# Kernel optimization log

Measured on AMD Instinct MI355X. Metric: run time of the kernel, lower is better.

## Reference

```python
import jax, jax.numpy as jnp
import numpy as np

B, T, D, H = 2, 2048, 1024, 16
DK = D // H


def setup_inputs() -> dict:
    key = jax.random.key(0)
    ks = jax.random.split(key, 11)
    s = 0.02
    inp = {
        "q": jax.random.normal(ks[0], (B, T, D), jnp.float32),
        "k": jax.random.normal(ks[1], (B, T, D), jnp.float32),
        "v": jax.random.normal(ks[2], (B, T, D), jnp.float32),
        # True = masked (causal), broadcast over batch and heads
        "attn_mask": jnp.triu(jnp.ones((T, T), bool), k=1)[None, None],
        "Wq": jax.random.normal(ks[3], (D, D), jnp.float32) * s,
        "bq": jnp.zeros((D,), jnp.float32),
        "Wk": jax.random.normal(ks[4], (D, D), jnp.float32) * s,
        "bk": jnp.zeros((D,), jnp.float32),
        "Wv": jax.random.normal(ks[5], (D, D), jnp.float32) * s,
        "bv": jnp.zeros((D,), jnp.float32),
        "Wo": jax.random.normal(ks[6], (D, D), jnp.float32) * s,
        "bo": jnp.zeros((D,), jnp.float32),
    }
    return inp


def _split_heads(x):
    # [B,T,D] -> [B,H,T,DK]
    return x.reshape(B, T, H, DK).transpose(0, 2, 1, 3)


def reference(q, k, v, attn_mask, Wq, bq, Wk, bk, Wv, bv, Wo, bo):
    query = _split_heads(q @ Wq.T + bq)
    key_ = _split_heads(k @ Wk.T + bk)
    value = _split_heads(v @ Wv.T + bv)
    scale = 1.0 / jnp.sqrt(jnp.asarray(DK, query.dtype))
    scores = jnp.einsum("bhqd,bhkd->bhqk", query, key_) * scale
    scores = jnp.where(attn_mask, -jnp.inf, scores)
    probs = jax.nn.softmax(scores, axis=-1)  # dropout p=0.0 (eval)
    ctx = jnp.einsum("bhqk,bhkd->bhqd", probs, value)
    ctx = ctx.transpose(0, 2, 1, 3).reshape(B, T, D)
    return ctx @ Wo.T + bo
```

## Files before the change

### kernel.cpp

```cpp
#include <hip/hip_runtime.h>
#include <stdint.h>

#define Bsz 2
#define Tseq 2048
#define Dmodel 1024
#define Hn 16
#define DKd 64

typedef __bf16 bf16;
typedef bf16 bf16x8 __attribute__((ext_vector_type(8)));
typedef float f32x4 __attribute__((ext_vector_type(4)));

__device__ inline void gld_lds16(const void* g, void* l) {
  __builtin_amdgcn_global_load_lds(
      (const __attribute__((address_space(1))) uint32_t*)g,
      (__attribute__((address_space(3))) uint32_t*)l, 16, 0, 0);
}

struct CvtArgs {
  const float* src[7];
  bf16* dst[7];
  int n4[7];
};

__global__ void __launch_bounds__(256) cvt_f32_bf16(CvtArgs a) {
  const int z = blockIdx.y;
  const float4* s = (const float4*)a.src[z];
  uint2* d = (uint2*)a.dst[z];
  const int n4 = a.n4[z];
  for (int i = blockIdx.x * 256 + threadIdx.x; i < n4; i += gridDim.x * 256) {
    float4 v = s[i];
    union { bf16 h[4]; uint2 u; } pk;
    pk.h[0] = (bf16)v.x; pk.h[1] = (bf16)v.y;
    pk.h[2] = (bf16)v.z; pk.h[3] = (bf16)v.w;
    d[i] = pk.u;
  }
}

struct GemmArgs {
  const bf16* A[3];
  const bf16* W[3];
  const float* bias[3];
  void* out[3];
  int mode[3];
  float scale[3];
};

__global__ void __launch_bounds__(256) gemm_bt(GemmArgs g) {
  const int z = blockIdx.z;
  const bf16* __restrict__ A = g.A[z];
  const bf16* __restrict__ W = g.W[z];
  const float* __restrict__ bias = g.bias[z];
  const int mode = g.mode[z];
  const float scl = g.scale[z];

  __shared__ __align__(16) bf16 As[128 * 32];
  __shared__ __align__(16) bf16 Bs[128 * 32];

  const int tid = threadIdx.x;
  const int w = tid >> 6, lane = tid & 63;
  const int l15 = lane & 15, quad = lane >> 4;
  const int wm = (w >> 1) * 64, wn = (w & 1) * 64;
  const int m0 = blockIdx.y * 128, n0 = blockIdx.x * 128;

  f32x4 zero = {0.f, 0.f, 0.f, 0.f};
  f32x4 acc[4][4];
#pragma unroll
  for (int mi = 0; mi < 4; ++mi)
#pragma unroll
    for (int ni = 0; ni < 4; ++ni) acc[mi][ni] = zero;

  for (int k0 = 0; k0 < Dmodel; k0 += 32) {
    __syncthreads();
#pragma unroll
    for (int p = 0; p < 2; ++p) {
      const int c = p * 256 + tid;
      const int row = c >> 2, ko = (c & 3) * 8;
      gld_lds16(A + (size_t)(m0 + row) * Dmodel + k0 + ko, (void*)(As + c * 8));
      gld_lds16(W + (size_t)(n0 + row) * Dmodel + k0 + ko, (void*)(Bs + c * 8));
    }
    __syncthreads();

    bf16x8 af[4], bfr[4];
#pragma unroll
    for (int i = 0; i < 4; ++i) {
      af[i]  = *(const bf16x8*)(As + (wm + i * 16 + l15) * 32 + quad * 8);
      bfr[i] = *(const bf16x8*)(Bs + (wn + i * 16 + l15) * 32 + quad * 8);
    }
#pragma unroll
    for (int mi = 0; mi < 4; ++mi)
#pragma unroll
      for (int ni = 0; ni < 4; ++ni)
        acc[mi][ni] = __builtin_amdgcn_mfma_f32_16x16x32_bf16(af[mi], bfr[ni],
                                                              acc[mi][ni], 0, 0, 0);
  }

#pragma unroll
  for (int mi = 0; mi < 4; ++mi) {
#pragma unroll
    for (int r = 0; r < 4; ++r) {
      const int m = m0 + wm + mi * 16 + quad * 4 + r;
      const int bb = m >> 11, tt = m & 2047;
#pragma unroll
      for (int ni = 0; ni < 4; ++ni) {
        const int n = n0 + wn + ni * 16 + l15;
        const float val = (acc[mi][ni][r] + bias[n]) * scl;
        if (mode == 0) {
          bf16* o = (bf16*)g.out[z];
          const int hh = n >> 6, dk = n & 63;
          o[((size_t)(bb * Hn + hh) * Tseq + tt) * DKd + dk] = (bf16)val;
        } else if (mode == 1) {
          bf16* o = (bf16*)g.out[z];
          const int hh = n >> 6, dk = n & 63;
          o[((size_t)(bb * Hn + hh) * DKd + dk) * Tseq + tt] = (bf16)val;
        } else {
          float* o = (float*)g.out[z];
          o[(size_t)m * Dmodel + n] = val;
        }
      }
    }
  }
}

__global__ void __launch_bounds__(256) gemm_out64(const bf16* __restrict__ A,
                                                  const bf16* __restrict__ W,
                                                  const float* __restrict__ bias,
                                                  float* __restrict__ out) {
  __shared__ __align__(16) bf16 As[64 * 32];
  __shared__ __align__(16) bf16 Bs[128 * 32];

  const int tid = threadIdx.x;
  const int w = tid >> 6, lane = tid & 63;
  const int l15 = lane & 15, quad = lane >> 4;
  const int wm = (w >> 1) * 32, wn = (w & 1) * 64;
  const int m0 = blockIdx.y * 64, n0 = blockIdx.x * 128;

  f32x4 zero = {0.f, 0.f, 0.f, 0.f};
  f32x4 acc[2][4];
#pragma unroll
  for (int mi = 0; mi < 2; ++mi)
#pragma unroll
    for (int ni = 0; ni < 4; ++ni) acc[mi][ni] = zero;

  for (int k0 = 0; k0 < Dmodel; k0 += 32) {
    __syncthreads();
    {
      const int c = tid;
      const int row = c >> 2, ko = (c & 3) * 8;
      gld_lds16(A + (size_t)(m0 + row) * Dmodel + k0 + ko, (void*)(As + c * 8));
    }
#pragma unroll
    for (int p = 0; p < 2; ++p) {
      const int c = p * 256 + tid;
      const int row = c >> 2, ko = (c & 3) * 8;
      gld_lds16(W + (size_t)(n0 + row) * Dmodel + k0 + ko, (void*)(Bs + c * 8));
    }
    __syncthreads();

    bf16x8 af[2], bfr[4];
#pragma unroll
    for (int i = 0; i < 2; ++i)
      af[i] = *(const bf16x8*)(As + (wm + i * 16 + l15) * 32 + quad * 8);
#pragma unroll
    for (int i = 0; i < 4; ++i)
      bfr[i] = *(const bf16x8*)(Bs + (wn + i * 16 + l15) * 32 + quad * 8);
#pragma unroll
    for (int mi = 0; mi < 2; ++mi)
#pragma unroll
      for (int ni = 0; ni < 4; ++ni)
        acc[mi][ni] = __builtin_amdgcn_mfma_f32_16x16x32_bf16(af[mi], bfr[ni],
                                                              acc[mi][ni], 0, 0, 0);
  }

#pragma unroll
  for (int mi = 0; mi < 2; ++mi)
#pragma unroll
    for (int r = 0; r < 4; ++r) {
      const int m = m0 + wm + mi * 16 + quad * 4 + r;
#pragma unroll
      for (int ni = 0; ni < 4; ++ni) {
        const int n = n0 + wn + ni * 16 + l15;
        out[(size_t)m * Dmodel + n] = acc[mi][ni][r] + bias[n];
      }
    }
}

__global__ void __launch_bounds__(256) attn_fused(const bf16* __restrict__ Q,
                                                  const bf16* __restrict__ K,
                                                  const bf16* __restrict__ Vt,
                                                  bf16* __restrict__ ctx) {
  __shared__ __align__(16) bf16 Ks[8 * 128 * 8];
  __shared__ __align__(16) bf16 Vs[16 * 64 * 8];
  __shared__ __align__(16) bf16 plds[4][16][136];

  const int tid = threadIdx.x;
  const int w = tid >> 6, lane = tid & 63;
  const int l15 = lane & 15, quad = lane >> 4;

  const int l = blockIdx.x;
  const int qt = (Tseq / 64 - 1) - (l >> 5);
  const int hb = l & 31;
  const int h = hb & 15, b = hb >> 4;
  const int bh = b * Hn + h;
  const int qb = qt * 64 + w * 16;

  const bf16* Qb = Q + (size_t)bh * Tseq * DKd;
  const bf16* Kb = K + (size_t)bh * Tseq * DKd;
  const bf16* Vb = Vt + (size_t)bh * DKd * Tseq;

  bf16x8 aq0 = *(const bf16x8*)(Qb + (size_t)(qb + l15) * DKd + quad * 8);
  bf16x8 aq1 = *(const bf16x8*)(Qb + (size_t)(qb + l15) * DKd + 32 + quad * 8);

  f32x4 zero = {0.f, 0.f, 0.f, 0.f};
  f32x4 oacc[4];
#pragma unroll
  for (int nd = 0; nd < 4; ++nd) oacc[nd] = zero;
  f32x4 lacc = zero;

  bf16x8 onesf;
#pragma unroll
  for (int i = 0; i < 8; ++i) onesf[i] = (bf16)1.0f;

  const int qmax = qt * 64 + 48;
  for (int j0 = 0; j0 <= qmax; j0 += 128) {
    __syncthreads();
#pragma unroll
    for (int p = 0; p < 4; ++p) {
      const int c = p * 256 + tid;
      gld_lds16(Kb + (size_t)(j0 + (c & 127)) * DKd + (c >> 7) * 8,
                (void*)(Ks + c * 8));
      gld_lds16(Vb + (size_t)(c & 63) * Tseq + j0 + (c >> 6) * 8,
                (void*)(Vs + c * 8));
    }
    __syncthreads();

    if (j0 <= qb) {
      f32x4 s[8];
#pragma unroll
      for (int ct = 0; ct < 8; ++ct) s[ct] = zero;
#pragma unroll
      for (int ct = 0; ct < 8; ++ct) {
        bf16x8 bk0 = *(const bf16x8*)(Ks + ((quad)*128 + ct * 16 + l15) * 8);
        bf16x8 bk1 = *(const bf16x8*)(Ks + ((4 + quad) * 128 + ct * 16 + l15) * 8);
        s[ct] = __builtin_amdgcn_mfma_f32_16x16x32_bf16(aq0, bk0, s[ct], 0, 0, 0);
        s[ct] = __builtin_amdgcn_mfma_f32_16x16x32_bf16(aq1, bk1, s[ct], 0, 0, 0);
      }

      if (j0 + 128 <= qb) {
#pragma unroll
        for (int r = 0; r < 4; ++r)
#pragma unroll
          for (int ct = 0; ct < 8; ++ct)
            plds[w][quad * 4 + r][ct * 16 + l15] = (bf16)exp2f(s[ct][r]);
      } else {
#pragma unroll
        for (int r = 0; r < 4; ++r) {
          const int qrow = qb + quad * 4 + r;
#pragma unroll
          for (int ct = 0; ct < 8; ++ct) {
            const int col = j0 + ct * 16 + l15;
            const float p = exp2f(s[ct][r]);
            plds[w][quad * 4 + r][ct * 16 + l15] = (bf16)((col <= qrow) ? p : 0.f);
          }
        }
      }

      bf16x8 ap[4];
#pragma unroll
      for (int kc = 0; kc < 4; ++kc)
        ap[kc] = *(const bf16x8*)(&plds[w][l15][kc * 32 + quad * 8]);

#pragma unroll
      for (int kc = 0; kc < 4; ++kc) {
        lacc = __builtin_amdgcn_mfma_f32_16x16x32_bf16(ap[kc], onesf, lacc, 0, 0, 0);
#pragma unroll
        for (int nd = 0; nd < 4; ++nd) {
          bf16x8 bv = *(const bf16x8*)(Vs + ((kc * 4 + quad) * 64 + nd * 16 + l15) * 8);
          oacc[nd] = __builtin_amdgcn_mfma_f32_16x16x32_bf16(ap[kc], bv, oacc[nd], 0, 0, 0);
        }
      }
    }
  }

  float inv[4];
#pragma unroll
  for (int r = 0; r < 4; ++r) inv[r] = 1.0f / lacc[r];
  bf16* cb = ctx + ((size_t)(b * Tseq + qb + quad * 4)) * Dmodel + h * DKd;
#pragma unroll
  for (int nd = 0; nd < 4; ++nd)
#pragma unroll
    for (int r = 0; r < 4; ++r)
      cb[(size_t)r * Dmodel + nd * 16 + l15] = (bf16)(oacc[nd][r] * inv[r]);
}

extern "C" void kernel_launch(void* const* d_in, const int* in_sizes, int n_in,
                              void* d_out, int out_size, void* d_ws, size_t ws_size,
                              hipStream_t stream) {
  const float* q = (const float*)d_in[0];
  const float* k = (const float*)d_in[1];
  const float* v = (const float*)d_in[2];
  const float* Wq = (const float*)d_in[4];
  const float* bq = (const float*)d_in[5];
  const float* Wk = (const float*)d_in[6];
  const float* bk = (const float*)d_in[7];
  const float* Wv = (const float*)d_in[8];
  const float* bv = (const float*)d_in[9];
  const float* Wo = (const float*)d_in[10];
  const float* bo = (const float*)d_in[11];

  char* ws = (char*)d_ws;
  const size_t MB = 1024 * 1024;
  bf16* Wq_b = (bf16*)(ws + 0 * MB);
  bf16* Wk_b = (bf16*)(ws + 2 * MB);
  bf16* Wv_b = (bf16*)(ws + 4 * MB);
  bf16* Wo_b = (bf16*)(ws + 6 * MB);
  bf16* q_b  = (bf16*)(ws + 8 * MB);
  bf16* k_b  = (bf16*)(ws + 16 * MB);
  bf16* v_b  = (bf16*)(ws + 24 * MB);
  bf16* Qh   = (bf16*)(ws + 32 * MB);
  bf16* Kh   = (bf16*)(ws + 40 * MB);
  bf16* Vt   = (bf16*)(ws + 48 * MB);
  bf16* ctx  = (bf16*)(ws + 8 * MB);

  const int NACT4 = (Bsz * Tseq * Dmodel) / 4;
  const int NW4 = (Dmodel * Dmodel) / 4;

  CvtArgs ca;
  ca.src[0] = q;  ca.dst[0] = q_b;  ca.n4[0] = NACT4;
  ca.src[1] = k;  ca.dst[1] = k_b;  ca.n4[1] = NACT4;
  ca.src[2] = v;  ca.dst[2] = v_b;  ca.n4[2] = NACT4;
  ca.src[3] = Wq; ca.dst[3] = Wq_b; ca.n4[3] = NW4;
  ca.src[4] = Wk; ca.dst[4] = Wk_b; ca.n4[4] = NW4;
  ca.src[5] = Wv; ca.dst[5] = Wv_b; ca.n4[5] = NW4;
  ca.src[6] = Wo; ca.dst[6] = Wo_b; ca.n4[6] = NW4;
  cvt_f32_bf16<<<dim3(512, 7), 256, 0, stream>>>(ca);

  const float SC = 0.125f * 1.4426950408889634f;
  GemmArgs ga;
  ga.A[0] = q_b; ga.W[0] = Wq_b; ga.bias[0] = bq; ga.out[0] = Qh; ga.mode[0] = 0; ga.scale[0] = SC;
  ga.A[1] = k_b; ga.W[1] = Wk_b; ga.bias[1] = bk; ga.out[1] = Kh; ga.mode[1] = 0; ga.scale[1] = 1.f;
  ga.A[2] = v_b; ga.W[2] = Wv_b; ga.bias[2] = bv; ga.out[2] = Vt; ga.mode[2] = 1; ga.scale[2] = 1.f;
  gemm_bt<<<dim3(Dmodel / 128, (Bsz * Tseq) / 128, 3), 256, 0, stream>>>(ga);

  attn_fused<<<dim3((Tseq / 64) * Hn * Bsz), 256, 0, stream>>>(Qh, Kh, Vt, ctx);

  gemm_out64<<<dim3(Dmodel / 128, (Bsz * Tseq) / 64), 256, 0, stream>>>(
      ctx, Wo_b, bo, (float*)d_out);
}
```

Baseline: 251.9 us.

## Fuse activation fp32-to-bf16 conversion into QKV GEMM and deepen K tile

The q/k/v activations are no longer converted to bf16 in a separate pass. The QKV GEMM now loads fp32 A tiles into registers, converts them to bf16 in flight and stores them into padded LDS, prefetching the next K slice while the current one computes. This removes the write and re-read of the bf16 activation copies. Both GEMMs also move from K=32 to K=64 per iteration, halving the barriers, and the conversion kernel now handles only the four weight matrices. In exchange, register pressure rises and fp32 loads double the global read width for A.

Result: slower. 270.2 us (+7.3%).

```diff
diff --git a/kernel.cpp b/kernel.cpp
--- a/kernel.cpp
+++ b/kernel.cpp
@@ -18,9 +18,9 @@
 }
 
 struct CvtArgs {
-  const float* src[7];
-  bf16* dst[7];
-  int n4[7];
+  const float* src[4];
+  bf16* dst[4];
+  int n4[4];
 };
 
 __global__ void __launch_bounds__(256) cvt_f32_bf16(CvtArgs a) {
@@ -38,7 +38,7 @@
 }
 
 struct GemmArgs {
-  const bf16* A[3];
+  const float* A[3];
   const bf16* W[3];
   const float* bias[3];
   void* out[3];
@@ -46,16 +46,16 @@
   float scale[3];
 };
 
-__global__ void __launch_bounds__(256) gemm_bt(GemmArgs g) {
+__global__ void __launch_bounds__(256) gemm_qkv(GemmArgs g) {
   const int z = blockIdx.z;
-  const bf16* __restrict__ A = g.A[z];
+  const float* __restrict__ A = g.A[z];
   const bf16* __restrict__ W = g.W[z];
   const float* __restrict__ bias = g.bias[z];
   const int mode = g.mode[z];
   const float scl = g.scale[z];
 
-  __shared__ __align__(16) bf16 As[128 * 32];
-  __shared__ __align__(16) bf16 Bs[128 * 32];
+  __shared__ __align__(16) bf16 As[2][128][40];
+  __shared__ __align__(16) bf16 Bs[2][128][32];
 
   const int tid = threadIdx.x;
   const int w = tid >> 6, lane = tid & 63;
@@ -70,29 +70,59 @@
 #pragma unroll
     for (int ni = 0; ni < 4; ++ni) acc[mi][ni] = zero;
 
-  for (int k0 = 0; k0 < Dmodel; k0 += 32) {
-    __syncthreads();
-#pragma unroll
-    for (int p = 0; p < 2; ++p) {
+  float4 pa[4][2];
+#define LOAD_A(k0v)                                                         \
+  {                                                                         \
+    _Pragma("unroll") for (int p = 0; p < 4; ++p) {                         \
+      const int gg = p * 256 + tid;                                         \
+      const int row = gg >> 3, cg = gg & 7;                                 \
+      const float4* src =                                                   \
+          (const float4*)(A + (size_t)(m0 + row) * Dmodel + (k0v) + cg * 8);\
+      pa[p][0] = src[0];                                                    \
+      pa[p][1] = src[1];                                                    \
+    }                                                                       \
+  }
+  LOAD_A(0)
+
+  for (int k0 = 0; k0 < Dmodel; k0 += 64) {
+    __syncthreads();
+#pragma unroll
+    for (int p = 0; p < 4; ++p) {
+      const int gg = p * 256 + tid;
+      const int row = gg >> 3, cg = gg & 7;
+      bf16x8 t;
+      t[0] = (bf16)pa[p][0].x; t[1] = (bf16)pa[p][0].y;
+      t[2] = (bf16)pa[p][0].z; t[3] = (bf16)pa[p][0].w;
+      t[4] = (bf16)pa[p][1].x; t[5] = (bf16)pa[p][1].y;
+      t[6] = (bf16)pa[p][1].z; t[7] = (bf16)pa[p][1].w;
+      *(bf16x8*)(&As[cg >> 2][row][(cg & 3) * 8]) = t;
+    }
+#pragma unroll
+    for (int p = 0; p < 4; ++p) {
       const int c = p * 256 + tid;
-      const int row = c >> 2, ko = (c & 3) * 8;
-      gld_lds16(A + (size_t)(m0 + row) * Dmodel + k0 + ko, (void*)(As + c * 8));
-      gld_lds16(W + (size_t)(n0 + row) * Dmodel + k0 + ko, (void*)(Bs + c * 8));
-    }
-    __syncthreads();
-
-    bf16x8 af[4], bfr[4];
-#pragma unroll
-    for (int i = 0; i < 4; ++i) {
-      af[i]  = *(const bf16x8*)(As + (wm + i * 16 + l15) * 32 + quad * 8);
-      bfr[i] = *(const bf16x8*)(Bs + (wn + i * 16 + l15) * 32 + quad * 8);
-    }
-#pragma unroll
-    for (int mi = 0; mi < 4; ++mi)
-#pragma unroll
-      for (int ni = 0; ni < 4; ++ni)
-        acc[mi][ni] = __builtin_amdgcn_mfma_f32_16x16x32_bf16(af[mi], bfr[ni],
-                                                              acc[mi][ni], 0, 0, 0);
+      const int half = c >> 9, row = (c >> 2) & 127, ko = (c & 3) * 8;
+      gld_lds16(W + (size_t)(n0 + row) * Dmodel + k0 + half * 32 + ko,
+                (void*)(&Bs[half][row][ko]));
+    }
+    const int k0n = (k0 + 64 < Dmodel) ? k0 + 64 : 0;
+    LOAD_A(k0n)
+    __syncthreads();
+
+#pragma unroll
+    for (int ks = 0; ks < 2; ++ks) {
+      bf16x8 af[4], bfr[4];
+#pragma unroll
+      for (int i = 0; i < 4; ++i) {
+        af[i]  = *(const bf16x8*)(&As[ks][wm + i * 16 + l15][quad * 8]);
+        bfr[i] = *(const bf16x8*)(&Bs[ks][wn + i * 16 + l15][quad * 8]);
+      }
+#pragma unroll
+      for (int mi = 0; mi < 4; ++mi)
+#pragma unroll
+        for (int ni = 0; ni < 4; ++ni)
+          acc[mi][ni] = __builtin_amdgcn_mfma_f32_16x16x32_bf16(
+              af[mi], bfr[ni], acc[mi][ni], 0, 0, 0);
+    }
   }
 
 #pragma unroll
@@ -105,17 +135,12 @@
       for (int ni = 0; ni < 4; ++ni) {
         const int n = n0 + wn + ni * 16 + l15;
         const float val = (acc[mi][ni][r] + bias[n]) * scl;
+        bf16* o = (bf16*)g.out[z];
+        const int hh = n >> 6, dk = n & 63;
         if (mode == 0) {
-          bf16* o = (bf16*)g.out[z];
-          const int hh = n >> 6, dk = n & 63;
           o[((size_t)(bb * Hn + hh) * Tseq + tt) * DKd + dk] = (bf16)val;
-        } else if (mode == 1) {
-          bf16* o = (bf16*)g.out[z];
-          const int hh = n >> 6, dk = n & 63;
+        } else {
           o[((size_t)(bb * Hn + hh) * DKd + dk) * Tseq + tt] = (bf16)val;
-        } else {
-          float* o = (float*)g.out[z];
-          o[(size_t)m * Dmodel + n] = val;
         }
       }
     }
@@ -126,8 +151,8 @@
                                                   const bf16* __restrict__ W,
                                                   const float* __restrict__ bias,
                                                   float* __restrict__ out) {
-  __shared__ __align__(16) bf16 As[64 * 32];
-  __shared__ __align__(16) bf16 Bs[128 * 32];
+  __shared__ __align__(16) bf16 As[2][64][32];
+  __shared__ __align__(16) bf16 Bs[2][128][32];
 
   const int tid = threadIdx.x;
   const int w = tid >> 6, lane = tid & 63;
@@ -142,34 +167,40 @@
 #pragma unroll
     for (int ni = 0; ni < 4; ++ni) acc[mi][ni] = zero;
 
-  for (int k0 = 0; k0 < Dmodel; k0 += 32) {
-    __syncthreads();
-    {
-      const int c = tid;
-      const int row = c >> 2, ko = (c & 3) * 8;
-      gld_lds16(A + (size_t)(m0 + row) * Dmodel + k0 + ko, (void*)(As + c * 8));
-    }
+  for (int k0 = 0; k0 < Dmodel; k0 += 64) {
+    __syncthreads();
 #pragma unroll
     for (int p = 0; p < 2; ++p) {
       const int c = p * 256 + tid;
-      const int row = c >> 2, ko = (c & 3) * 8;
-      gld_lds16(W + (size_t)(n0 + row) * Dmodel + k0 + ko, (void*)(Bs + c * 8));
-    }
-    __syncthreads();
-
-    bf16x8 af[2], bfr[4];
-#pragma unroll
-    for (int i = 0; i < 2; ++i)
-      af[i] = *(const bf16x8*)(As + (wm + i * 16 + l15) * 32 + quad * 8);
-#pragma unroll
-    for (int i = 0; i < 4; ++i)
-      bfr[i] = *(const bf16x8*)(Bs + (wn + i * 16 + l15) * 32 + quad * 8);
-#pragma unroll
-    for (int mi = 0; mi < 2; ++mi)
-#pragma unroll
-      for (int ni = 0; ni < 4; ++ni)
-        acc[mi][ni] = __builtin_amdgcn_mfma_f32_16x16x32_bf16(af[mi], bfr[ni],
-                                                              acc[mi][ni], 0, 0, 0);
+      const int half = c >> 8, row = (c >> 2) & 63, ko = (c & 3) * 8;
+      gld_lds16(A + (size_t)(m0 + row) * Dmodel + k0 + half * 32 + ko,
+                (void*)(&As[half][row][ko]));
+    }
+#pragma unroll
+    for (int p = 0; p < 4; ++p) {
+      const int c = p * 256 + tid;
+      const int half = c >> 9, row = (c >> 2) & 127, ko = (c & 3) * 8;
+      gld_lds16(W + (size_t)(n0 + row) * Dmodel + k0 + half * 32 + ko,
+                (void*)(&Bs[half][row][ko]));
+    }
+    __syncthreads();
+
+#pragma unroll
+    for (int ks = 0; ks < 2; ++ks) {
+      bf16x8 af[2], bfr[4];
+#pragma unroll
+      for (int i = 0; i < 2; ++i)
+        af[i] = *(const bf16x8*)(&As[ks][wm + i * 16 + l15][quad * 8]);
+#pragma unroll
+      for (int i = 0; i < 4; ++i)
+        bfr[i] = *(const bf16x8*)(&Bs[ks][wn + i * 16 + l15][quad * 8]);
+#pragma unroll
+      for (int mi = 0; mi < 2; ++mi)
+#pragma unroll
+        for (int ni = 0; ni < 4; ++ni)
+          acc[mi][ni] = __builtin_amdgcn_mfma_f32_16x16x32_bf16(
+              af[mi], bfr[ni], acc[mi][ni], 0, 0, 0);
+    }
   }
 
 #pragma unroll
@@ -314,33 +345,26 @@
   bf16* Wk_b = (bf16*)(ws + 2 * MB);
   bf16* Wv_b = (bf16*)(ws + 4 * MB);
   bf16* Wo_b = (bf16*)(ws + 6 * MB);
-  bf16* q_b  = (bf16*)(ws + 8 * MB);
-  bf16* k_b  = (bf16*)(ws + 16 * MB);
-  bf16* v_b  = (bf16*)(ws + 24 * MB);
+  bf16* ctx  = (bf16*)(ws + 8 * MB);
   bf16* Qh   = (bf16*)(ws + 32 * MB);
   bf16* Kh   = (bf16*)(ws + 40 * MB);
   bf16* Vt   = (bf16*)(ws + 48 * MB);
-  bf16* ctx  = (bf16*)(ws + 8 * MB);
-
-  const int NACT4 = (Bsz * Tseq * Dmodel) / 4;
+
   const int NW4 = (Dmodel * Dmodel) / 4;
 
   CvtArgs ca;
-  ca.src[0] = q;  ca.dst[0] = q_b;  ca.n4[0] = NACT4;
-  ca.src[1] = k;  ca.dst[1] = k_b;  ca.n4[1] = NACT4;
-  ca.src[2] = v;  ca.dst[2] = v_b;  ca.n4[2] = NACT4;
-  ca.src[3] = Wq; ca.dst[3] = Wq_b; ca.n4[3] = NW4;
-  ca.src[4] = Wk; ca.dst[4] = Wk_b; ca.n4[4] = NW4;
-  ca.src[5] = Wv; ca.dst[5] = Wv_b; ca.n4[5] = NW4;
-  ca.src[6] = Wo; ca.dst[6] = Wo_b; ca.n4[6] = NW4;
-  cvt_f32_bf16<<<dim3(512, 7), 256, 0, stream>>>(ca);
+  ca.src[0] = Wq; ca.dst[0] = Wq_b; ca.n4[0] = NW4;
+  ca.src[1] = Wk; ca.dst[1] = Wk_b; ca.n4[1] = NW4;
+  ca.src[2] = Wv; ca.dst[2] = Wv_b; ca.n4[2] = NW4;
+  ca.src[3] = Wo; ca.dst[3] = Wo_b; ca.n4[3] = NW4;
+  cvt_f32_bf16<<<dim3(128, 4), 256, 0, stream>>>(ca);
 
   const float SC = 0.125f * 1.4426950408889634f;
   GemmArgs ga;
-  ga.A[0] = q_b; ga.W[0] = Wq_b; ga.bias[0] = bq; ga.out[0] = Qh; ga.mode[0] = 0; ga.scale[0] = SC;
-  ga.A[1] = k_b; ga.W[1] = Wk_b; ga.bias[1] = bk; ga.out[1] = Kh; ga.mode[1] = 0; ga.scale[1] = 1.f;
-  ga.A[2] = v_b; ga.W[2] = Wv_b; ga.bias[2] = bv; ga.out[2] = Vt; ga.mode[2] = 1; ga.scale[2] = 1.f;
-  gemm_bt<<<dim3(Dmodel / 128, (Bsz * Tseq) / 128, 3), 256, 0, stream>>>(ga);
+  ga.A[0] = q; ga.W[0] = Wq_b; ga.bias[0] = bq; ga.out[0] = Qh; ga.mode[0] = 0; ga.scale[0] = SC;
+  ga.A[1] = k; ga.W[1] = Wk_b; ga.bias[1] = bk; ga.out[1] = Kh; ga.mode[1] = 0; ga.scale[1] = 1.f;
+  ga.A[2] = v; ga.W[2] = Wv_b; ga.bias[2] = bv; ga.out[2] = Vt; ga.mode[2] = 1; ga.scale[2] = 1.f;
+  gemm_qkv<<<dim3(Dmodel / 128, (Bsz * Tseq) / 128, 3), 256, 0, stream>>>(ga);
 
   attn_fused<<<dim3((Tseq / 64) * Hn * Bsz), 256, 0, stream>>>(Qh, Kh, Vt, ctx);
 
```
